# Kernel optimization log

Measured on AMD Instinct MI355X. Metric: run time of the kernel, lower is better.

The kernel has to match this reference:

```python
import jax, jax.numpy as jnp
import numpy as np

DIM = 768
HID = 3072
E_SPEC = 4
E_SHARED = 2
TOP_K = 2
LN_EPS = 1e-5


def _expert_stack_params(key, n_experts):
    k1, k2, k3, k4 = jax.random.split(key, 4)
    s1 = 1.0 / np.sqrt(DIM)
    s2 = 1.0 / np.sqrt(HID)
    return {
        'w1': jax.random.uniform(k1, (n_experts, DIM, HID), minval=-s1, maxval=s1, dtype=jnp.float32),
        'b1': jax.random.uniform(k2, (n_experts, HID), minval=-s1, maxval=s1, dtype=jnp.float32),
        'w2': jax.random.uniform(k3, (n_experts, HID, DIM), minval=-s2, maxval=s2, dtype=jnp.float32),
        'b2': jax.random.uniform(k4, (n_experts, DIM), minval=-s2, maxval=s2, dtype=jnp.float32),
    }


def setup_inputs() -> dict:
    key = jax.random.key(0)
    ks = jax.random.split(key, 8)
    B, N = 64, 196
    s = 1.0 / np.sqrt(DIM)
    spec = _expert_stack_params(ks[1], E_SPEC)
    shared = _expert_stack_params(ks[2], E_SHARED)
    return {
        'x': jax.random.normal(ks[0], (B, N, DIM), dtype=jnp.float32),
        'ln_gamma': jnp.ones((DIM,), jnp.float32),
        'ln_beta': jnp.zeros((DIM,), jnp.float32),
        'spec_router_w': jax.random.uniform(ks[3], (DIM, E_SPEC), minval=-s, maxval=s, dtype=jnp.float32),
        'spec_router_b': jnp.zeros((E_SPEC,), jnp.float32),
        'spec_w1': spec['w1'], 'spec_b1': spec['b1'], 'spec_w2': spec['w2'], 'spec_b2': spec['b2'],
        'shared_router_w': jax.random.uniform(ks[4], (DIM, E_SHARED), minval=-s, maxval=s, dtype=jnp.float32),
        'shared_router_b': jnp.zeros((E_SHARED,), jnp.float32),
        'sh_w1': shared['w1'], 'sh_b1': shared['b1'], 'sh_w2': shared['w2'], 'sh_b2': shared['b2'],
    }


def _all_experts(x, w1, b1, w2, b2):
    # x: [B,N,D]; w1: [E,D,H] -> out: [B,N,E,D]
    h = jnp.einsum('bnd,edh->bneh', x, w1) + b1
    h = jax.nn.gelu(h, approximate=False)  # torch nn.GELU default is exact
    return jnp.einsum('bneh,ehd->bned', h, w2) + b2


def reference(x, ln_gamma, ln_beta,
              spec_router_w, spec_router_b, spec_w1, spec_b1, spec_w2, spec_b2,
              shared_router_w, shared_router_b, sh_w1, sh_b1, sh_w2, sh_b2):
    # LayerNorm
    mu = jnp.mean(x, axis=-1, keepdims=True)
    var = jnp.mean(jnp.square(x - mu), axis=-1, keepdims=True)
    xn = (x - mu) * jax.lax.rsqrt(var + LN_EPS) * ln_gamma + ln_beta

    # Specific-expert branch: dense all-expert compute, then top-k gather (faithful)
    spec_logits = xn @ spec_router_w + spec_router_b            # [B,N,E]
    spec_probs = jax.nn.softmax(spec_logits, axis=-1)
    topk_probs, topk_idx = jax.lax.top_k(spec_probs, TOP_K)    # [B,N,K]
    spec_out_all = _all_experts(xn, spec_w1, spec_b1, spec_w2, spec_b2)  # [B,N,E,D]
    sel = jnp.take_along_axis(spec_out_all, topk_idx[..., None], axis=2)  # [B,N,K,D]
    specific_out = jnp.sum(topk_probs[..., None] * sel, axis=2)

    # Shared-expert branch: softmax-weighted sum over all experts
    sh_logits = xn @ shared_router_w + shared_router_b          # [B,N,Es]
    sh_probs = jax.nn.softmax(sh_logits, axis=-1)
    sh_out_all = _all_experts(xn, sh_w1, sh_b1, sh_w2, sh_b2)   # [B,N,Es,D]
    shared_out = jnp.einsum('bne,bned->bnd', sh_probs, sh_out_all)

    out = specific_out + shared_out
    return (out, spec_logits, spec_probs, topk_idx, topk_probs, sh_logits, sh_probs)
```

## Files before the change

kernel.cpp:

```cpp
#include <hip/hip_runtime.h>
#include <hip/hip_bf16.h>
#include <math.h>

#define NTOK 12544
#define DIM 768
#define HID 3072
#define NTILE_MAX 102
#define NSLOT_MAX (NTILE_MAX * 256)
#define NSDT 49
#define NVT (NTILE_MAX + 2 * NSDT)
#define NBKT 64
#define BKTCAP 256
#define LDSB 131072

typedef __hip_bfloat16 bf16;
typedef __attribute__((ext_vector_type(8))) short short8v;
typedef __attribute__((ext_vector_type(4))) float f32x4;

#define GPTR(p)  ((const __attribute__((address_space(1))) void*)(p))
#define LDSPTR(p) ((__attribute__((address_space(3))) void*)(p))

__global__ __launch_bounds__(256) void conv_all_kernel(
    const float* __restrict__ spec_w1, const float* __restrict__ sh_w1,
    const float* __restrict__ spec_w2, const float* __restrict__ sh_w2,
    bf16* __restrict__ w1t, bf16* __restrict__ w2t,
    int* __restrict__ cnt2, int* __restrict__ slot_tok, float* __restrict__ slot_gate) {
    int z = blockIdx.y;
    int ti = blockIdx.x;
    int t = threadIdx.x;
    if (z == 0) {
        if (ti == 0) cnt2[t] = 0;
        if (ti < NTILE_MAX) {
            int s = ti * 256 + t;
            slot_tok[s] = 0; slot_gate[s] = 0.0f;
        }
    }
    const float* src; bf16* dst; int R, C, tr, tc;
    if (z < 6) {
        R = DIM; C = HID;
        src = (z < 4) ? spec_w1 + (size_t)z * R * C : sh_w1 + (size_t)(z - 4) * R * C;
        dst = w1t + (size_t)z * R * C;
        tr = ti % 12; tc = ti / 12;
    } else {
        int e = z - 6;
        R = HID; C = DIM;
        src = (e < 4) ? spec_w2 + (size_t)e * R * C : sh_w2 + (size_t)(e - 4) * R * C;
        dst = w2t + (size_t)e * R * C;
        tr = ti % 48; tc = ti / 48;
    }
    __shared__ float tile[64][65];
    int r0 = tr * 64, c0 = tc * 64;
    int lr = t >> 4, lc = (t & 15) * 4;
    #pragma unroll
    for (int ii = 0; ii < 4; ++ii) {
        float4 v = *(const float4*)&src[(size_t)(r0 + lr + 16 * ii) * C + c0 + lc];
        tile[lc + 0][lr + 16 * ii] = v.x;
        tile[lc + 1][lr + 16 * ii] = v.y;
        tile[lc + 2][lr + 16 * ii] = v.z;
        tile[lc + 3][lr + 16 * ii] = v.w;
    }
    __syncthreads();
    int oc = t >> 4, orr = (t & 15) * 4;
    #pragma unroll
    for (int ii = 0; ii < 4; ++ii) {
        union { ushort4 u4; bf16 h[4]; } pk;
        #pragma unroll
        for (int k = 0; k < 4; ++k)
            pk.h[k] = __float2bfloat16(tile[oc + 16 * ii][orr + k]);
        *(ushort4*)&dst[(size_t)(c0 + oc + 16 * ii) * R + r0 + orr] = pk.u4;
    }
}

__global__ void router_ln_kernel(const float* __restrict__ x,
                                 const float* __restrict__ lng, const float* __restrict__ lnb,
                                 const float* __restrict__ srw, const float* __restrict__ srb,
                                 const float* __restrict__ shw, const float* __restrict__ shb,
                                 bf16* __restrict__ xnb,
                                 float* __restrict__ spec_logits, float* __restrict__ spec_probs,
                                 float* __restrict__ topk_idx, float* __restrict__ topk_probs,
                                 float* __restrict__ sh_logits, float* __restrict__ sh_probs,
                                 float* __restrict__ gates,
                                 int* __restrict__ cnt2, int* __restrict__ tok2,
                                 float* __restrict__ gate2) {
    int t = blockIdx.x * 4 + (threadIdx.x >> 6);
    int bucket = blockIdx.x & (NBKT - 1);
    int lane = threadIdx.x & 63;
    const float* xr = x + (size_t)t * DIM;
    bf16* xb = xnb + (size_t)t * DIM;
    float v[12];
    float s = 0.0f;
    #pragma unroll
    for (int i = 0; i < 6; ++i) {
        float2 xv = *(const float2*)&xr[lane * 2 + 128 * i];
        v[2 * i] = xv.x; v[2 * i + 1] = xv.y;
        s += xv.x + xv.y;
    }
    #pragma unroll
    for (int o = 32; o > 0; o >>= 1) s += __shfl_xor(s, o, 64);
    float mean = s * (1.0f / 768.0f);
    float sq = 0.0f;
    #pragma unroll
    for (int i = 0; i < 12; ++i) { float d = v[i] - mean; sq += d * d; }
    #pragma unroll
    for (int o = 32; o > 0; o >>= 1) sq += __shfl_xor(sq, o, 64);
    float rstd = rsqrtf(sq * (1.0f / 768.0f) + 1e-5f);

    float acc[6] = {0, 0, 0, 0, 0, 0};
    #pragma unroll
    for (int i = 0; i < 6; ++i) {
        int d0 = lane * 2 + 128 * i;
        float xn0 = (v[2 * i]     - mean) * rstd * lng[d0]     + lnb[d0];
        float xn1 = (v[2 * i + 1] - mean) * rstd * lng[d0 + 1] + lnb[d0 + 1];
        union { unsigned u; bf16 h[2]; } pk;
        pk.h[0] = __float2bfloat16(xn0);
        pk.h[1] = __float2bfloat16(xn1);
        *(unsigned*)&xb[d0] = pk.u;
        float4 a = *(const float4*)&srw[d0 * 4];
        float4 b = *(const float4*)&srw[d0 * 4 + 4];
        acc[0] += xn0 * a.x + xn1 * b.x;
        acc[1] += xn0 * a.y + xn1 * b.y;
        acc[2] += xn0 * a.z + xn1 * b.z;
        acc[3] += xn0 * a.w + xn1 * b.w;
        float4 sw = *(const float4*)&shw[d0 * 2];
        acc[4] += xn0 * sw.x + xn1 * sw.z;
        acc[5] += xn0 * sw.y + xn1 * sw.w;
    }
    #pragma unroll
    for (int j = 0; j < 6; ++j) {
        #pragma unroll
        for (int o = 32; o > 0; o >>= 1) acc[j] += __shfl_xor(acc[j], o, 64);
    }
    if (lane == 0) {
        float l[4];
        #pragma unroll
        for (int j = 0; j < 4; ++j) l[j] = acc[j] + srb[j];
        float m = fmaxf(fmaxf(l[0], l[1]), fmaxf(l[2], l[3]));
        float e[4], ssum = 0.0f;
        #pragma unroll
        for (int j = 0; j < 4; ++j) { e[j] = expf(l[j] - m); ssum += e[j]; }
        float inv = 1.0f / ssum;
        float p[4];
        #pragma unroll
        for (int j = 0; j < 4; ++j) p[j] = e[j] * inv;
        int i0 = 0;
        for (int j = 1; j < 4; ++j) if (p[j] > p[i0]) i0 = j;
        int i1 = -1;
        for (int j = 0; j < 4; ++j) {
            if (j == i0) continue;
            if (i1 < 0 || p[j] > p[i1]) i1 = j;
        }
        float sl0 = acc[4] + shb[0], sl1 = acc[5] + shb[1];
        float sm = fmaxf(sl0, sl1);
        float se0 = expf(sl0 - sm), se1 = expf(sl1 - sm);
        float sinv = 1.0f / (se0 + se1);
        float sp0 = se0 * sinv, sp1 = se1 * sinv;

        #pragma unroll
        for (int j = 0; j < 4; ++j) {
            spec_logits[t * 4 + j] = l[j];
            spec_probs[t * 4 + j]  = p[j];
        }
        topk_idx[t * 2 + 0]   = (float)i0;
        topk_idx[t * 2 + 1]   = (float)i1;
        topk_probs[t * 2 + 0] = p[i0];
        topk_probs[t * 2 + 1] = p[i1];
        sh_logits[t * 2 + 0]  = sl0;
        sh_logits[t * 2 + 1]  = sl1;
        sh_probs[t * 2 + 0]   = sp0;
        sh_probs[t * 2 + 1]   = sp1;
        float gg[6] = {0, 0, 0, 0, sp0, sp1};
        gg[i0] = p[i0];
        gg[i1] = p[i1];
        #pragma unroll
        for (int j = 0; j < 6; ++j) gates[t * 6 + j] = gg[j];
        int c0 = i0 * NBKT + bucket;
        int pos0 = atomicAdd(&cnt2[c0], 1);
        tok2[c0 * BKTCAP + pos0]  = t * 2 + 0;
        gate2[c0 * BKTCAP + pos0] = p[i0];
        int c1 = i1 * NBKT + bucket;
        int pos1 = atomicAdd(&cnt2[c1], 1);
        tok2[c1 * BKTCAP + pos1]  = t * 2 + 1;
        gate2[c1 * BKTCAP + pos1] = p[i1];
    }
}

__global__ void plan_kernel(const int* __restrict__ cnt2, int* __restrict__ e_of_tile,
                            const int* __restrict__ tok2, const float* __restrict__ gate2,
                            int* __restrict__ slot_tok, float* __restrict__ slot_gate,
                            int* __restrict__ back) {
    __shared__ int sbase[4 * NBKT];
    __shared__ int offsE[5];
    __shared__ int etot[4];
    int tid = threadIdx.x, lane = tid & 63, wid = tid >> 6;
    int c = cnt2[wid * NBKT + lane];
    int inc = c;
    #pragma unroll
    for (int o = 1; o < 64; o <<= 1) {
        int tv = __shfl_up(inc, o, 64);
        if (lane >= o) inc += tv;
    }
    int exc = inc - c;
    if (lane == 63) etot[wid] = inc;
    __syncthreads();
    if (tid == 0) {
        int o = 0;
        for (int e = 0; e < 4; ++e) { offsE[e] = o; o += (etot[e] + 255) & ~255; }
        offsE[4] = o;
    }
    __syncthreads();
    sbase[tid] = offsE[wid] + exc;
    for (int idx = tid; idx < NTILE_MAX; idx += 256) {
        int s0 = idx * 256, e = -1;
        for (int j = 0; j < 4; ++j)
            if (s0 >= offsE[j] && s0 < offsE[j + 1]) e = j;
        e_of_tile[idx] = e;
    }
    __syncthreads();
    int bs = sbase[tid];
    int cc = cnt2[tid];
    for (int i = 0; i < cc; ++i) {
        int gs = bs + i;
        int tk = tok2[tid * BKTCAP + i];
        slot_tok[gs] = tk >> 1;
        slot_gate[gs] = gate2[tid * BKTCAP + i];
        back[tk] = gs;
    }
}

__global__ void gather_kernel(const bf16* __restrict__ xnb, const int* __restrict__ slot_tok,
                              bf16* __restrict__ xg) {
    int idx = blockIdx.x * 256 + threadIdx.x;
    int slot = idx / 96;
    int c = (idx % 96) * 8;
    int tok = slot_tok[slot];
    *(short8v*)&xg[(size_t)slot * DIM + c] = *(const short8v*)&xnb[(size_t)tok * DIM + c];
}

__device__ __forceinline__ int swz(int off) {
    return off ^ (((off >> 8) & 1) << 4) ^ (((off >> 9) & 1) << 5);
}

__device__ __forceinline__ void stage2(bf16* lds, int base_elems, int wid,
                                       const bf16* s0, const bf16* s1) {
    __builtin_amdgcn_global_load_lds(GPTR(s0), LDSPTR(lds + base_elems + wid * 512), 16, 0, 0);
    __builtin_amdgcn_global_load_lds(GPTR(s1), LDSPTR(lds + base_elems + 4096 + wid * 512), 16, 0, 0);
}

__device__ __forceinline__ void read_a4(const bf16* lds, int buf, int ks, int wm, int mh,
                                        int lane, short8v a[4]) {
    const char* base = (const char*)lds + buf * 32768 + ks * 16384;
    #pragma unroll
    for (int i = 0; i < 4; ++i) {
        int off = (wm * 128 + mh * 64 + i * 16 + (lane & 15)) * 64 + ((lane >> 4) * 16);
        a[i] = *(const short8v*)(base + swz(off));
    }
}

__device__ __forceinline__ void read_b4(const bf16* lds, int buf, int ks, int wn,
                                        int lane, short8v b[4]) {
    const char* base = (const char*)lds + 65536 + buf * 32768 + ks * 16384;
    #pragma unroll
    for (int j = 0; j < 4; ++j) {
        int off = (wn * 64 + j * 16 + (lane & 15)) * 64 + ((lane >> 4) * 16);
        b[j] = *(const short8v*)(base + swz(off));
    }
}

__device__ __forceinline__ void mfma16(const short8v a[4], const short8v b[4], f32x4 (*am)[4]) {
    #pragma unroll
    for (int i = 0; i < 4; ++i)
        #pragma unroll
        for (int j = 0; j < 4; ++j)
            am[i][j] = __builtin_amdgcn_mfma_f32_16x16x32_bf16(a[i], b[j], am[i][j], 0, 0, 0);
}

#define BARRIER() __builtin_amdgcn_s_barrier()
#define VMCNT4() asm volatile("s_waitcnt vmcnt(4)" ::: "memory")
#define VMCNT0() asm volatile("s_waitcnt vmcnt(0)" ::: "memory")

template<int NT>
__device__ __forceinline__ void kloop8p(bf16* lds, const bf16* a0, const bf16* a1,
                                        const bf16* b0, const bf16* b1,
                                        int wm, int wn, int wid, int lane,
                                        f32x4 acc[8][4]) {
    stage2(lds, 0, wid, a0, a1);
    stage2(lds, 32768, wid, b0, b1);
    stage2(lds, 8192, wid, a0 + 32, a1 + 32);
    stage2(lds, 32768 + 8192, wid, b0 + 32, b1 + 32);
    VMCNT4();
    BARRIER();
    for (int t = 0; t < NT; ++t) {
        int buf = t & 1, nb = buf ^ 1;
        bool pre = (t + 1 < NT);
        short8v af[4], bfv[4];
        if (pre) stage2(lds, nb * 16384, wid, a0 + (t + 1) * 64, a1 + (t + 1) * 64);
        read_a4(lds, buf, 0, wm, 0, lane, af);
        read_b4(lds, buf, 0, wn, lane, bfv);
        BARRIER();
        __builtin_amdgcn_s_setprio(1);
        mfma16(af, bfv, &acc[0]);
        __builtin_amdgcn_s_setprio(0);
        BARRIER();
        if (pre) stage2(lds, 32768 + nb * 16384, wid, b0 + (t + 1) * 64, b1 + (t + 1) * 64);
        read_a4(lds, buf, 0, wm, 1, lane, af);
        BARRIER();
        __builtin_amdgcn_s_setprio(1);
        mfma16(af, bfv, &acc[4]);
        __builtin_amdgcn_s_setprio(0);
        if (pre) VMCNT4(); else VMCNT0();
        BARRIER();
        if (pre) stage2(lds, nb * 16384 + 8192, wid, a0 + (t + 1) * 64 + 32, a1 + (t + 1) * 64 + 32);
        read_a4(lds, buf, 1, wm, 0, lane, af);
        read_b4(lds, buf, 1, wn, lane, bfv);
        BARRIER();
        __builtin_amdgcn_s_setprio(1);
        mfma16(af, bfv, &acc[0]);
        __builtin_amdgcn_s_setprio(0);
        BARRIER();
        if (pre) stage2(lds, 32768 + nb * 16384 + 8192, wid, b0 + (t + 1) * 64 + 32, b1 + (t + 1) * 64 + 32);
        read_a4(lds, buf, 1, wm, 1, lane, af);
        BARRIER();
        __builtin_amdgcn_s_setprio(1);
        mfma16(af, bfv, &acc[4]);
        __builtin_amdgcn_s_setprio(0);
        if (pre) VMCNT4();
        BARRIER();
    }
}

__device__ __forceinline__ float gelu_exact(float v) {
    return 0.5f * v * (1.0f + erff(v * 0.70710678118654752f));
}

__device__ __forceinline__ float gelu_fast(float x) {
    float z = 0.70710678118654752f * x;
    float az = fabsf(z);
    float t = __builtin_amdgcn_rcpf(1.0f + 0.3275911f * az);
    float poly = t * (0.254829592f + t * (-0.284496736f + t * (1.421413741f +
                 t * (-1.453152027f + t * 1.061405429f))));
    float erfv = 1.0f - poly * __expf(-az * az);
    erfv = (z < 0.0f) ? -erfv : erfv;
    return 0.5f * x * (1.0f + erfv);
}

__global__ __launch_bounds__(512, 2) void gemm1_8p(
    const bf16* __restrict__ xg, const bf16* __restrict__ xnb,
    const bf16* __restrict__ w1t,
    const float* __restrict__ spec_b1, const float* __restrict__ sh_b1,
    const int* __restrict__ e_of_tile,
    bf16* __restrict__ Hbuf, int y_base) {
    extern __shared__ bf16 lds[];
    int bx = blockIdx.x, by = blockIdx.y;
    int y = by + y_base;
    int tid = threadIdx.x, wid = tid >> 6, lane = tid & 63;
    int wm = wid >> 2, wn = wid & 3;
    int P0c = tid, P1c = 512 + tid;
    int L0 = P0c ^ ((P0c >> 4) & 1) ^ (((P0c >> 5) & 1) << 1);
    int L1 = P1c ^ ((P1c >> 4) & 1) ^ (((P1c >> 5) & 1) << 1);
    int r0 = L0 >> 2, c0 = (L0 & 3) * 8;
    int r1 = L1 >> 2, c1 = (L1 & 3) * 8;

    const bf16 *abase, *Bw;
    const float* bias;
    if (y < NTILE_MAX) {
        int e = e_of_tile[y];
        if (e < 0) return;
        abase = xg + (size_t)y * 256 * DIM;
        Bw = w1t + (size_t)e * HID * DIM;
        bias = spec_b1 + (size_t)e * HID;
    } else {
        int ys = y - NTILE_MAX;
        int z = ys / NSDT, ry = ys % NSDT;
        abase = xnb + (size_t)ry * 256 * DIM;
        Bw = w1t + (size_t)(4 + z) * HID * DIM;
        bias = sh_b1 + (size_t)z * HID;
    }
    const bf16* a0 = abase + (size_t)r0 * DIM + c0;
    const bf16* a1 = abase + (size_t)r1 * DIM + c1;
    const bf16* b0 = Bw + (size_t)(bx * 256 + r0) * DIM + c0;
    const bf16* b1 = Bw + (size_t)(bx * 256 + r1) * DIM + c1;

    f32x4 acc[8][4] = {};
    kloop8p<DIM / 64>(lds, a0, a1, b0, b1, wm, wn, wid, lane, acc);

    bf16* hb = Hbuf + (size_t)by * 256 * HID;
    int fr = lane & 15, fq = lane >> 4;
    int cb = bx * 256 + wn * 64;
    #pragma unroll
    for (int j = 0; j < 4; ++j) {
        int col = cb + j * 16 + fr;
        float bv = bias[col];
        #pragma unroll
        for (int ii = 0; ii < 8; ++ii) {
            #pragma unroll
            for (int rr = 0; rr < 4; ++rr) {
                int row = wm * 128 + (ii >> 2) * 64 + (ii & 3) * 16 + fq * 4 + rr;
                hb[(size_t)row * HID + col] = __float2bfloat16(gelu_fast(acc[ii][j][rr] + bv));
            }
        }
    }
}

__global__ __launch_bounds__(512, 2) void gemm2_8p(
    const bf16* __restrict__ Hbuf, const bf16* __restrict__ w2t,
    const float* __restrict__ spec_b2, const float* __restrict__ sh_b2,
    const int* __restrict__ e_of_tile, const float* __restrict__ slot_gate,
    const float* __restrict__ sh_probs,
    bf16* __restrict__ spec_g, bf16* __restrict__ shg, int y_base) {
    extern __shared__ bf16 lds[];
    int bx = blockIdx.x, by = blockIdx.y;
    int y = by + y_base;
    int tid = threadIdx.x, wid = tid >> 6, lane = tid & 63;
    int wm = wid >> 2, wn = wid & 3;
    int P0c = tid, P1c = 512 + tid;
    int L0 = P0c ^ ((P0c >> 4) & 1) ^ (((P0c >> 5) & 1) << 1);
    int L1 = P1c ^ ((P1c >> 4) & 1) ^ (((P1c >> 5) & 1) << 1);
    int r0 = L0 >> 2, c0 = (L0 & 3) * 8;
    int r1 = L1 >> 2, c1 = (L1 & 3) * 8;

    const bf16 *Bw;
    const float* bias;
    bf16* obase;
    bool grouped = (y < NTILE_MAX);
    int z = 0, ry = 0;
    if (grouped) {
        int e = e_of_tile[y];
        if (e < 0) return;
        Bw = w2t + (size_t)e * DIM * HID;
        bias = spec_b2 + (size_t)e * DIM;
        obase = spec_g + (size_t)y * 256 * DIM;
    } else {
        int ys = y - NTILE_MAX;
        z = ys / NSDT; ry = ys % NSDT;
        Bw = w2t + (size_t)(4 + z) * DIM * HID;
        bias = sh_b2 + (size_t)z * DIM;
        obase = shg + (size_t)(z * NTOK + ry * 256) * DIM;
    }
    const bf16* Ah = Hbuf + (size_t)by * 256 * HID;
    const bf16* a0 = Ah + (size_t)r0 * HID + c0;
    const bf16* a1 = Ah + (size_t)r1 * HID + c1;
    const bf16* b0 = Bw + (size_t)(bx * 256 + r0) * HID + c0;
    const bf16* b1 = Bw + (size_t)(bx * 256 + r1) * HID + c1;

    f32x4 acc[8][4] = {};
    kloop8p<HID / 64>(lds, a0, a1, b0, b1, wm, wn, wid, lane, acc);

    int fr = lane & 15, fq = lane >> 4;
    int cb = bx * 256 + wn * 64;
    #pragma unroll
    for (int j = 0; j < 4; ++j) {
        int col = cb + j * 16 + fr;
        float bv = bias[col];
        #pragma unroll
        for (int ii = 0; ii < 8; ++ii) {
            #pragma unroll
            for (int rr = 0; rr < 4; ++rr) {
                int row = wm * 128 + (ii >> 2) * 64 + (ii & 3) * 16 + fq * 4 + rr;
                float g = grouped ? slot_gate[y * 256 + row]
                                  : sh_probs[(size_t)(ry * 256 + row) * 2 + z];
                obase[(size_t)row * DIM + col] = __float2bfloat16(g * (acc[ii][j][rr] + bv));
            }
        }
    }
}

__device__ __forceinline__ void stage_tile(const bf16* __restrict__ g, int ldg,
                                           bf16* lds, int tid) {
    int wave = tid >> 6, lane = tid & 63;
    #pragma unroll
    for (int q = 0; q < 2; ++q) {
        int chunk = wave * 2 + q;
        int row = chunk * 16 + (lane >> 2);
        int col = (lane & 3) * 8;
        __builtin_amdgcn_global_load_lds(GPTR(g + (size_t)row * ldg + col),
                                         LDSPTR(lds + chunk * 512), 16, 0, 0);
    }
}

__device__ __forceinline__ void mfma_step(const bf16* As, const bf16* Bs,
                                          int wr, int wc, int fr, int fq, f32x4 acc[4][4]) {
    short8v a[4], b[4];
    #pragma unroll
    for (int i = 0; i < 4; ++i) {
        a[i] = *(const short8v*)&As[(wr * 64 + i * 16 + fr) * 32 + fq * 8];
        b[i] = *(const short8v*)&Bs[(wc * 64 + i * 16 + fr) * 32 + fq * 8];
    }
    #pragma unroll
    for (int i = 0; i < 4; ++i)
        #pragma unroll
        for (int j = 0; j < 4; ++j)
            acc[i][j] = __builtin_amdgcn_mfma_f32_16x16x32_bf16(a[i], b[j], acc[i][j], 0, 0, 0);
}

__global__ __launch_bounds__(256) void gemm1_dense(
    const bf16* __restrict__ A, const bf16* __restrict__ BT,
    const float* __restrict__ bias, bf16* __restrict__ H) {
    __shared__ bf16 As[128 * 32];
    __shared__ bf16 Bs[128 * 32];
    int tid = threadIdx.x;
    int wid = tid >> 6, lane = tid & 63;
    int wr = wid >> 1, wc = wid & 1;
    int fr = lane & 15, fq = lane >> 4;
    const bf16* Ag = A + (size_t)(blockIdx.y * 128) * DIM;
    const bf16* Bg = BT + (size_t)(blockIdx.x * 128) * DIM;
    f32x4 acc[4][4] = {};
    for (int k0 = 0; k0 < DIM; k0 += 32) {
        stage_tile(Ag + k0, DIM, As, tid);
        stage_tile(Bg + k0, DIM, Bs, tid);
        __syncthreads();
        mfma_step(As, Bs, wr, wc, fr, fq, acc);
        __syncthreads();
    }
    int rbase = blockIdx.y * 128 + wr * 64;
    int cbase = blockIdx.x * 128 + wc * 64;
    #pragma unroll
    for (int j = 0; j < 4; ++j) {
        int col = cbase + j * 16 + fr;
        float bv = bias[col];
        #pragma unroll
        for (int i = 0; i < 4; ++i)
            #pragma unroll
            for (int r = 0; r < 4; ++r) {
                int row = rbase + i * 16 + fq * 4 + r;
                H[(size_t)row * HID + col] = __float2bfloat16(gelu_exact(acc[i][j][r] + bv));
            }
    }
}

__global__ __launch_bounds__(256) void gemm2_dense_out(
    const bf16* __restrict__ A, const bf16* __restrict__ BT,
    const float* __restrict__ bias, const float* __restrict__ gates,
    float* __restrict__ out, int gidx, int accum) {
    __shared__ bf16 As[128 * 32];
    __shared__ bf16 Bs[128 * 32];
    int tid = threadIdx.x;
    int wid = tid >> 6, lane = tid & 63;
    int wr = wid >> 1, wc = wid & 1;
    int fr = lane & 15, fq = lane >> 4;
    const bf16* Ag = A + (size_t)(blockIdx.y * 128) * HID;
    const bf16* Bg = BT + (size_t)(blockIdx.x * 128) * HID;
    f32x4 acc[4][4] = {};
    for (int k0 = 0; k0 < HID; k0 += 32) {
        stage_tile(Ag + k0, HID, As, tid);
        stage_tile(Bg + k0, HID, Bs, tid);
        __syncthreads();
        mfma_step(As, Bs, wr, wc, fr, fq, acc);
        __syncthreads();
    }
    int rbase = blockIdx.y * 128 + wr * 64;
    int cbase = blockIdx.x * 128 + wc * 64;
    #pragma unroll
    for (int j = 0; j < 4; ++j) {
        int col = cbase + j * 16 + fr;
        float bv = bias[col];
        #pragma unroll
        for (int i = 0; i < 4; ++i)
            #pragma unroll
            for (int r = 0; r < 4; ++r) {
                int row = rbase + i * 16 + fq * 4 + r;
                float g = gates[(size_t)row * 6 + gidx];
                float v = g * (acc[i][j][r] + bv);
                size_t idx = (size_t)row * DIM + col;
                out[idx] = accum ? out[idx] + v : v;
            }
    }
}

__global__ void combine_kernel(const bf16* __restrict__ spec_g, const bf16* __restrict__ shg,
                               const int* __restrict__ back, float* __restrict__ out) {
    int idx = blockIdx.x * 256 + threadIdx.x;
    int tok = idx / 96;
    int c = (idx % 96) * 8;
    int b0 = back[2 * tok], b1 = back[2 * tok + 1];
    short8v q0 = *(const short8v*)&spec_g[(size_t)b0 * DIM + c];
    short8v q1 = *(const short8v*)&spec_g[(size_t)b1 * DIM + c];
    short8v s0 = *(const short8v*)&shg[(size_t)tok * DIM + c];
    short8v s1 = *(const short8v*)&shg[(size_t)(NTOK + tok) * DIM + c];
    float o[8];
    #pragma unroll
    for (int k = 0; k < 8; ++k) {
        float f0 = __uint_as_float((unsigned)(unsigned short)q0[k] << 16);
        float f1 = __uint_as_float((unsigned)(unsigned short)q1[k] << 16);
        float f2 = __uint_as_float((unsigned)(unsigned short)s0[k] << 16);
        float f3 = __uint_as_float((unsigned)(unsigned short)s1[k] << 16);
        o[k] = f0 + f1 + f2 + f3;
    }
    float* op = out + (size_t)tok * DIM + c;
    *(float4*)(op)     = *(const float4*)(o);
    *(float4*)(op + 4) = *(const float4*)(o + 4);
}

static inline size_t align256(size_t x) { return (x + 255) & ~(size_t)255; }

extern "C" void kernel_launch(void* const* d_in, const int* in_sizes, int n_in,
                              void* d_out, int out_size, void* d_ws, size_t ws_size,
                              hipStream_t stream) {
    const float* x      = (const float*)d_in[0];
    const float* gamma  = (const float*)d_in[1];
    const float* beta   = (const float*)d_in[2];
    const float* srw    = (const float*)d_in[3];
    const float* srb    = (const float*)d_in[4];
    const float* spec_w1 = (const float*)d_in[5];
    const float* spec_b1 = (const float*)d_in[6];
    const float* spec_w2 = (const float*)d_in[7];
    const float* spec_b2 = (const float*)d_in[8];
    const float* shw    = (const float*)d_in[9];
    const float* shb    = (const float*)d_in[10];
    const float* sh_w1  = (const float*)d_in[11];
    const float* sh_b1  = (const float*)d_in[12];
    const float* sh_w2  = (const float*)d_in[13];
    const float* sh_b2  = (const float*)d_in[14];

    char* p = (char*)d_ws;
    size_t off = 0;
    bf16* xnb = (bf16*)(p + off);       off = align256(off + (size_t)NTOK * DIM * 2);
    bf16* w1t = (bf16*)(p + off);       off = align256(off + (size_t)6 * HID * DIM * 2);
    bf16* w2t = (bf16*)(p + off);       off = align256(off + (size_t)6 * DIM * HID * 2);
    int*  cnt2 = (int*)(p + off);       off = align256(off + (size_t)4 * NBKT * 4);
    float* gates = (float*)(p + off);   off = align256(off + (size_t)NTOK * 6 * 4);
    int*  tok2 = (int*)(p + off);       off = align256(off + (size_t)4 * NBKT * BKTCAP * 4);
    float* gate2 = (float*)(p + off);   off = align256(off + (size_t)4 * NBKT * BKTCAP * 4);
    int*  slot_tok = (int*)(p + off);   off = align256(off + (size_t)NSLOT_MAX * 4);
    float* slot_gate = (float*)(p + off); off = align256(off + (size_t)NSLOT_MAX * 4);
    int*  back = (int*)(p + off);       off = align256(off + (size_t)2 * NTOK * 4);
    int*  e_of_tile = (int*)(p + off);  off = align256(off + (size_t)NTILE_MAX * 4);
    bf16* spec_g = (bf16*)(p + off);    off = align256(off + (size_t)NSLOT_MAX * DIM * 2);
    bf16* shg   = (bf16*)(p + off);     off = align256(off + (size_t)2 * NTOK * DIM * 2);
    size_t fixed_end = off;
    bf16* Hbuf = (bf16*)(p + fixed_end);
    bf16* xg = spec_g;

    const size_t tile_bytes = (size_t)256 * HID * 2;
    size_t avail = (ws_size > fixed_end) ? (ws_size - fixed_end) : 0;
    int tcap = (int)(avail / tile_bytes);
    if (tcap > NVT) tcap = NVT;

    float* out         = (float*)d_out;
    float* spec_logits = out + (size_t)NTOK * DIM;
    float* spec_probs  = spec_logits + (size_t)NTOK * 4;
    float* topk_idx    = spec_probs  + (size_t)NTOK * 4;
    float* topk_probs  = topk_idx    + (size_t)NTOK * 2;
    float* sh_logits   = topk_probs  + (size_t)NTOK * 2;
    float* sh_probs    = sh_logits   + (size_t)NTOK * 2;

    conv_all_kernel<<<dim3(576, 12), 256, 0, stream>>>(
        spec_w1, sh_w1, spec_w2, sh_w2, w1t, w2t, cnt2, slot_tok, slot_gate);

    router_ln_kernel<<<NTOK / 4, 256, 0, stream>>>(x, gamma, beta, srw, srb, shw, shb, xnb,
                                                   spec_logits, spec_probs, topk_idx,
                                                   topk_probs, sh_logits, sh_probs, gates,
                                                   cnt2, tok2, gate2);

    if (tcap >= 8) {
        plan_kernel<<<1, 256, 0, stream>>>(cnt2, e_of_tile, tok2, gate2,
                                           slot_tok, slot_gate, back);
        gather_kernel<<<NSLOT_MAX * 96 / 256, 256, 0, stream>>>(xnb, slot_tok, xg);
        int nch = (NVT + tcap - 1) / tcap;
        int csz = (NVT + nch - 1) / nch;
        for (int c0 = 0; c0 < NVT; c0 += csz) {
            int n = NVT - c0 < csz ? NVT - c0 : csz;
            gemm1_8p<<<dim3(HID / 256, n), 512, LDSB, stream>>>(
                xg, xnb, w1t, spec_b1, sh_b1, e_of_tile, Hbuf, c0);
            gemm2_8p<<<dim3(DIM / 256, n), 512, LDSB, stream>>>(
                Hbuf, w2t, spec_b2, sh_b2, e_of_tile, slot_gate, sh_probs,
                spec_g, shg, c0);
        }
        combine_kernel<<<NTOK * 96 / 256, 256, 0, stream>>>(spec_g, shg, back, out);
    } else {
        bf16* HB = spec_g;
        for (int e = 0; e < 6; ++e) {
            const bf16* w1p = w1t + (size_t)e * HID * DIM;
            const bf16* w2p = w2t + (size_t)e * DIM * HID;
            const float* b1p = (e < 4) ? spec_b1 + (size_t)e * HID : sh_b1 + (size_t)(e - 4) * HID;
            const float* b2p = (e < 4) ? spec_b2 + (size_t)e * DIM : sh_b2 + (size_t)(e - 4) * DIM;
            gemm1_dense<<<dim3(HID / 128, NTOK / 128), 256, 0, stream>>>(xnb, w1p, b1p, HB);
            gemm2_dense_out<<<dim3(DIM / 128, NTOK / 128), 256, 0, stream>>>(
                HB, w2p, b2p, gates, out, e, e > 0);
        }
    }
}
```

Baseline: 903.0 us.

## Split gemm1 into 128-row tiles with 48KB LDS for higher occupancy

Replaces the 256x256 gemm1 tile kernel with a 128x256 variant that uses a simpler two-stage double-buffered K loop over 32-wide slices and only 48KB of LDS, so up to four blocks can reside per CU. Each virtual tile is now split into two halves along the token dimension, doubling the grid. The host chunking of virtual tiles is also reworked to use different chunk sizes. The aim is better latency hiding and load balance in the first GEMM, at the cost of less per-block data reuse, since each B tile is loaded twice, and more barrier overhead per unit of work.

Result: faster. 839.6 us (-7.0%).

```diff
diff --git a/kernel.cpp b/kernel.cpp
--- a/kernel.cpp
+++ b/kernel.cpp
@@ -12,6 +12,7 @@
 #define NBKT 64
 #define BKTCAP 256
 #define LDSB 131072
+#define LDSB1 49152
 
 typedef __hip_bfloat16 bf16;
 typedef __attribute__((ext_vector_type(8))) short short8v;
@@ -246,6 +247,19 @@
     __builtin_amdgcn_global_load_lds(GPTR(s1), LDSPTR(lds + base_elems + 4096 + wid * 512), 16, 0, 0);
 }
 
+__device__ __forceinline__ void mfma16(const short8v a[4], const short8v b[4], f32x4 (*am)[4]) {
+    #pragma unroll
+    for (int i = 0; i < 4; ++i)
+        #pragma unroll
+        for (int j = 0; j < 4; ++j)
+            am[i][j] = __builtin_amdgcn_mfma_f32_16x16x32_bf16(a[i], b[j], am[i][j], 0, 0, 0);
+}
+
+#define BARRIER() __builtin_amdgcn_s_barrier()
+#define VMCNT4() asm volatile("s_waitcnt vmcnt(4)" ::: "memory")
+#define VMCNT3() asm volatile("s_waitcnt vmcnt(3)" ::: "memory")
+#define VMCNT0() asm volatile("s_waitcnt vmcnt(0)" ::: "memory")
+
 __device__ __forceinline__ void read_a4(const bf16* lds, int buf, int ks, int wm, int mh,
                                         int lane, short8v a[4]) {
     const char* base = (const char*)lds + buf * 32768 + ks * 16384;
@@ -265,18 +279,6 @@
         b[j] = *(const short8v*)(base + swz(off));
     }
 }
-
-__device__ __forceinline__ void mfma16(const short8v a[4], const short8v b[4], f32x4 (*am)[4]) {
-    #pragma unroll
-    for (int i = 0; i < 4; ++i)
-        #pragma unroll
-        for (int j = 0; j < 4; ++j)
-            am[i][j] = __builtin_amdgcn_mfma_f32_16x16x32_bf16(a[i], b[j], am[i][j], 0, 0, 0);
-}
-
-#define BARRIER() __builtin_amdgcn_s_barrier()
-#define VMCNT4() asm volatile("s_waitcnt vmcnt(4)" ::: "memory")
-#define VMCNT0() asm volatile("s_waitcnt vmcnt(0)" ::: "memory")
 
 template<int NT>
 __device__ __forceinline__ void kloop8p(bf16* lds, const bf16* a0, const bf16* a1,
@@ -328,6 +330,53 @@
     }
 }
 
+__device__ __forceinline__ void read_a4_128(const bf16* lds, int cur, int wm,
+                                            int lane, short8v a[4]) {
+    const char* base = (const char*)lds + cur * 8192;
+    #pragma unroll
+    for (int i = 0; i < 4; ++i) {
+        int off = (wm * 64 + i * 16 + (lane & 15)) * 64 + ((lane >> 4) * 16);
+        a[i] = *(const short8v*)(base + swz(off));
+    }
+}
+
+__device__ __forceinline__ void read_b4_128(const bf16* lds, int cur, int wn,
+                                            int lane, short8v b[4]) {
+    const char* base = (const char*)lds + 16384 + cur * 16384;
+    #pragma unroll
+    for (int j = 0; j < 4; ++j) {
+        int off = (wn * 64 + j * 16 + (lane & 15)) * 64 + ((lane >> 4) * 16);
+        b[j] = *(const short8v*)(base + swz(off));
+    }
+}
+
+template<int NS>
+__device__ __forceinline__ void kloop2p(bf16* lds, const bf16* aA,
+                                        const bf16* b0, const bf16* b1,
+                                        int wm, int wn, int wid, int lane,
+                                        f32x4 acc[4][4]) {
+    __builtin_amdgcn_global_load_lds(GPTR(aA), LDSPTR(lds + wid * 512), 16, 0, 0);
+    stage2(lds, 8192, wid, b0, b1);
+    for (int s = 0; s < NS; ++s) {
+        int cur = s & 1, nb = cur ^ 1;
+        bool pre = (s + 1 < NS);
+        if (pre) {
+            __builtin_amdgcn_global_load_lds(GPTR(aA + (s + 1) * 32),
+                                             LDSPTR(lds + nb * 4096 + wid * 512), 16, 0, 0);
+            stage2(lds, 8192 + nb * 8192, wid, b0 + (s + 1) * 32, b1 + (s + 1) * 32);
+        }
+        if (pre) VMCNT3(); else VMCNT0();
+        BARRIER();
+        short8v av[4], bv[4];
+        read_a4_128(lds, cur, wm, lane, av);
+        read_b4_128(lds, cur, wn, lane, bv);
+        __builtin_amdgcn_s_setprio(1);
+        mfma16(av, bv, &acc[0]);
+        __builtin_amdgcn_s_setprio(0);
+        BARRIER();
+    }
+}
+
 __device__ __forceinline__ float gelu_exact(float v) {
     return 0.5f * v * (1.0f + erff(v * 0.70710678118654752f));
 }
@@ -343,7 +392,7 @@
     return 0.5f * x * (1.0f + erfv);
 }
 
-__global__ __launch_bounds__(512, 2) void gemm1_8p(
+__global__ __launch_bounds__(512, 4) void gemm1_2p(
     const bf16* __restrict__ xg, const bf16* __restrict__ xnb,
     const bf16* __restrict__ w1t,
     const float* __restrict__ spec_b1, const float* __restrict__ sh_b1,
@@ -351,39 +400,42 @@
     bf16* __restrict__ Hbuf, int y_base) {
     extern __shared__ bf16 lds[];
     int bx = blockIdx.x, by = blockIdx.y;
-    int y = by + y_base;
+    int lt = by >> 1, half = by & 1;
+    int y = y_base + lt;
     int tid = threadIdx.x, wid = tid >> 6, lane = tid & 63;
     int wm = wid >> 2, wn = wid & 3;
+    int PA = tid;
+    int LA = PA ^ ((PA >> 4) & 1) ^ (((PA >> 5) & 1) << 1);
+    int ra = LA >> 2, ca = (LA & 3) * 8;
     int P0c = tid, P1c = 512 + tid;
     int L0 = P0c ^ ((P0c >> 4) & 1) ^ (((P0c >> 5) & 1) << 1);
     int L1 = P1c ^ ((P1c >> 4) & 1) ^ (((P1c >> 5) & 1) << 1);
-    int r0 = L0 >> 2, c0 = (L0 & 3) * 8;
-    int r1 = L1 >> 2, c1 = (L1 & 3) * 8;
+    int rb0 = L0 >> 2, cb0 = (L0 & 3) * 8;
+    int rb1 = L1 >> 2, cb1 = (L1 & 3) * 8;
 
     const bf16 *abase, *Bw;
     const float* bias;
     if (y < NTILE_MAX) {
         int e = e_of_tile[y];
         if (e < 0) return;
-        abase = xg + (size_t)y * 256 * DIM;
+        abase = xg + (size_t)(y * 256 + half * 128) * DIM;
         Bw = w1t + (size_t)e * HID * DIM;
         bias = spec_b1 + (size_t)e * HID;
     } else {
         int ys = y - NTILE_MAX;
         int z = ys / NSDT, ry = ys % NSDT;
-        abase = xnb + (size_t)ry * 256 * DIM;
+        abase = xnb + (size_t)(ry * 256 + half * 128) * DIM;
         Bw = w1t + (size_t)(4 + z) * HID * DIM;
         bias = sh_b1 + (size_t)z * HID;
     }
-    const bf16* a0 = abase + (size_t)r0 * DIM + c0;
-    const bf16* a1 = abase + (size_t)r1 * DIM + c1;
-    const bf16* b0 = Bw + (size_t)(bx * 256 + r0) * DIM + c0;
-    const bf16* b1 = Bw + (size_t)(bx * 256 + r1) * DIM + c1;
-
-    f32x4 acc[8][4] = {};
-    kloop8p<DIM / 64>(lds, a0, a1, b0, b1, wm, wn, wid, lane, acc);
-
-    bf16* hb = Hbuf + (size_t)by * 256 * HID;
+    const bf16* aA = abase + (size_t)ra * DIM + ca;
+    const bf16* b0 = Bw + (size_t)(bx * 256 + rb0) * DIM + cb0;
+    const bf16* b1 = Bw + (size_t)(bx * 256 + rb1) * DIM + cb1;
+
+    f32x4 acc[4][4] = {};
+    kloop2p<DIM / 32>(lds, aA, b0, b1, wm, wn, wid, lane, acc);
+
+    bf16* hb = Hbuf + (size_t)(lt * 256 + half * 128) * HID;
     int fr = lane & 15, fq = lane >> 4;
     int cb = bx * 256 + wn * 64;
     #pragma unroll
@@ -391,11 +443,11 @@
         int col = cb + j * 16 + fr;
         float bv = bias[col];
         #pragma unroll
-        for (int ii = 0; ii < 8; ++ii) {
+        for (int i = 0; i < 4; ++i) {
             #pragma unroll
             for (int rr = 0; rr < 4; ++rr) {
-                int row = wm * 128 + (ii >> 2) * 64 + (ii & 3) * 16 + fq * 4 + rr;
-                hb[(size_t)row * HID + col] = __float2bfloat16(gelu_fast(acc[ii][j][rr] + bv));
+                int row = wm * 64 + i * 16 + fq * 4 + rr;
+                hb[(size_t)row * HID + col] = __float2bfloat16(gelu_fast(acc[i][j][rr] + bv));
             }
         }
     }
@@ -655,11 +707,11 @@
         plan_kernel<<<1, 256, 0, stream>>>(cnt2, e_of_tile, tok2, gate2,
                                            slot_tok, slot_gate, back);
         gather_kernel<<<NSLOT_MAX * 96 / 256, 256, 0, stream>>>(xnb, slot_tok, xg);
-        int nch = (NVT + tcap - 1) / tcap;
-        int csz = (NVT + nch - 1) / nch;
+        int csz = tcap >= 67 ? (NVT + 2) / 3 : (tcap < 64 ? tcap : 64);
+        if (csz > tcap) csz = tcap;
         for (int c0 = 0; c0 < NVT; c0 += csz) {
             int n = NVT - c0 < csz ? NVT - c0 : csz;
-            gemm1_8p<<<dim3(HID / 256, n), 512, LDSB, stream>>>(
+            gemm1_2p<<<dim3(HID / 256, 2 * n), 512, LDSB1, stream>>>(
                 xg, xnb, w1t, spec_b1, sh_b1, e_of_tile, Hbuf, c0);
             gemm2_8p<<<dim3(DIM / 256, n), 512, LDSB, stream>>>(
                 Hbuf, w2t, spec_b2, sh_b2, e_of_tile, slot_gate, sh_probs,
```
